# Optimization experiments

Hardware: AMD Instinct MI355X
Metric: run time of the kernel (lower is better)

Reference implementation:

```python
import jax, jax.numpy as jnp
import numpy as np

N = 50000   # num_nodes
D = 128     # h_dim
R = 32      # num_rels * 2 (forward + inverse relations)
B = 8       # num_bases
E = 600000  # num_edges


def setup_inputs() -> dict:
    key = jax.random.key(0)
    ks = jax.random.split(key, 14)
    s = 1.0 / np.sqrt(D)
    return {
        "h_ids": jnp.arange(N, dtype=jnp.int32),
        "src": jax.random.randint(ks[0], (E,), 0, N),
        "dst": jax.random.randint(ks[1], (E,), 0, N),
        "etype": jax.random.randint(ks[2], (E,), 0, R),
        "norm": jax.random.uniform(ks[3], (E, 1), dtype=jnp.float32),
        "embedding": jax.random.normal(ks[4], (N, D), dtype=jnp.float32) * 0.05,
        "w_comp1": jax.random.normal(ks[5], (R, B), dtype=jnp.float32) * (1.0 / np.sqrt(B)),
        "bases1": jax.random.normal(ks[6], (B, D, D), dtype=jnp.float32) * s,
        "loop_w1": jax.random.normal(ks[7], (D, D), dtype=jnp.float32) * s,
        "bias1": jnp.zeros((D,), dtype=jnp.float32),
        "w_comp2": jax.random.normal(ks[8], (R, B), dtype=jnp.float32) * (1.0 / np.sqrt(B)),
        "bases2": jax.random.normal(ks[9], (B, D, D), dtype=jnp.float32) * s,
        "loop_w2": jax.random.normal(ks[10], (D, D), dtype=jnp.float32) * s,
        "bias2": jnp.zeros((D,), dtype=jnp.float32),
    }


def _rel_graph_conv(h, src, dst, etype, norm, w_comp, bases, loop_w, bias, act):
    # basis decomposition: W[r] = sum_b w_comp[r,b] * bases[b]
    W = jnp.einsum('rb,bio->rio', w_comp, bases)          # [R, D, D]
    # transform every node by every relation weight (dense GEMM)
    all_t = jnp.einsum('ni,rio->nro', h, W)               # [N, R, D]
    # per-edge gather of relation-specific transformed source features
    msg = all_t[src, etype] * norm                        # [E, D]
    # scatter-aggregate messages at destination nodes
    agg = jax.ops.segment_sum(msg, dst, num_segments=h.shape[0])  # [N, D]
    out = agg + h @ loop_w + bias                         # self-loop + bias
    return act(out) if act is not None else out


def reference(h_ids, src, dst, etype, norm, embedding,
              w_comp1, bases1, loop_w1, bias1,
              w_comp2, bases2, loop_w2, bias2):
    # EmbeddingLayer
    h = embedding[h_ids]                                  # [N, D]
    # hidden layer 0: relu activation (idx < num_hidden_layers-1)
    h = _rel_graph_conv(h, src, dst, etype, norm, w_comp1, bases1, loop_w1, bias1, jax.nn.relu)
    # hidden layer 1: no activation (last layer)
    h = _rel_graph_conv(h, src, dst, etype, norm, w_comp2, bases2, loop_w2, bias2, None)
    return h
```

## Files before the change

kernel.cpp:

```cpp
#include <hip/hip_runtime.h>

#define DD 128
#define NB 8
#define KTOT 1152

typedef unsigned int uint_t;
typedef __attribute__((ext_vector_type(8))) _Float16 half8v;
typedef __attribute__((ext_vector_type(2))) _Float16 half2v;
typedef __attribute__((ext_vector_type(4))) float f32x4;

static __device__ __forceinline__ void gld_lds16(const _Float16* g, _Float16* l)
{
  __builtin_amdgcn_global_load_lds(
      (const __attribute__((address_space(1))) void*)g,
      (__attribute__((address_space(3))) void*)l, 16, 0, 0);
}

static __device__ __forceinline__ half2v bc_h2(uint_t u)
{
  union { uint_t u; half2v h; } c; c.u = u; return c.h;
}

static __device__ __forceinline__ float fdot2(uint_t a, uint_t b, float acc)
{
#if __has_builtin(__builtin_amdgcn_fdot2)
  return __builtin_amdgcn_fdot2(bc_h2(a), bc_h2(b), acc, false);
#else
  half2v x = bc_h2(a), y = bc_h2(b);
  return acc + (float)x[0] * (float)y[0] + (float)x[1] * (float)y[1];
#endif
}

__global__ __launch_bounds__(256) void k_prep_w(
    const float* __restrict__ bases1, const float* __restrict__ loopw1,
    const float* __restrict__ bases2, const float* __restrict__ loopw2,
    _Float16* __restrict__ WcA)
{
  int i = blockIdx.x * 256 + threadIdx.x;
  if (i >= 2 * 36 * DD * 32) return;
  int layer = i / (36 * DD * 32);
  int rem   = i % (36 * DD * 32);
  int ks    = rem / (DD * 32);
  int rem2  = rem % (DD * 32);
  int feat  = rem2 / 32;
  int j     = rem2 % 32;
  int k     = ks * 32 + j;
  const float* basesL = layer ? bases2 : bases1;
  const float* loopwL = layer ? loopw2 : loopw1;
  float v;
  if (k < 1024) {
    int kk = k >> 3, b = k & 7;
    v = basesL[((size_t)b * DD + kk) * DD + feat];
  } else {
    v = loopwL[(size_t)(k - 1024) * DD + feat];
  }
  WcA[i] = (_Float16)v;
}

__global__ __launch_bounds__(256) void k_cast(
    const float* __restrict__ h, const int* __restrict__ ids,
    _Float16* __restrict__ hf, int N)
{
  int i = blockIdx.x * 256 + threadIdx.x;
  if (i >= N * (DD / 8)) return;
  int n  = i / (DD / 8);
  int k8 = (i % (DD / 8)) * 8;
  int row = ids ? ids[n] : n;
  const float* hp = h + (size_t)row * DD + k8;
  float4 v0 = *(const float4*)hp;
  float4 v1 = *(const float4*)(hp + 4);
  union { _Float16 e[8]; uint4 q; } p;
  p.e[0]=(_Float16)v0.x; p.e[1]=(_Float16)v0.y; p.e[2]=(_Float16)v0.z; p.e[3]=(_Float16)v0.w;
  p.e[4]=(_Float16)v1.x; p.e[5]=(_Float16)v1.y; p.e[6]=(_Float16)v1.z; p.e[7]=(_Float16)v1.w;
  *(uint4*)&hf[(size_t)n * DD + k8] = p.q;
}

__global__ __launch_bounds__(256) void k_zero(int* __restrict__ p, int n)
{
  int i = blockIdx.x * 256 + threadIdx.x;
  if (i < n) p[i] = 0;
}

__global__ __launch_bounds__(256) void k_fill(int* __restrict__ p, int val, int n)
{
  int i = blockIdx.x * 256 + threadIdx.x;
  if (i < n) p[i] = val;
}

__global__ __launch_bounds__(256) void k_hist(
    const int* __restrict__ dst, int* __restrict__ cnt, int E)
{
  int e = blockIdx.x * 256 + threadIdx.x;
  if (e < E) atomicAdd(&cnt[dst[e]], 1);
}

__global__ __launch_bounds__(256) void k_bsum(
    const int* __restrict__ cnt, int* __restrict__ bsum, int N)
{
  __shared__ int s[256];
  int i = blockIdx.x * 256 + threadIdx.x;
  s[threadIdx.x] = (i < N) ? ((cnt[i] + 1) & ~1) : 0;
  __syncthreads();
  for (int off = 128; off > 0; off >>= 1) {
    if (threadIdx.x < off) s[threadIdx.x] += s[threadIdx.x + off];
    __syncthreads();
  }
  if (threadIdx.x == 0) bsum[blockIdx.x] = s[0];
}

__global__ __launch_bounds__(256) void k_scanb(
    const int* __restrict__ bsum, int* __restrict__ boff, int nb)
{
  __shared__ int s[256];
  int t = threadIdx.x;
  int own = (t < nb) ? bsum[t] : 0;
  s[t] = own;
  __syncthreads();
  for (int off = 1; off < 256; off <<= 1) {
    int v = (t >= off) ? s[t - off] : 0;
    __syncthreads();
    s[t] += v;
    __syncthreads();
  }
  if (t < nb) boff[t] = s[t] - own;
}

__global__ __launch_bounds__(256) void k_scan3(
    const int* __restrict__ cnt, const int* __restrict__ boff,
    int* __restrict__ row_start, int N)
{
  __shared__ int s[256];
  int t = threadIdx.x;
  int i = blockIdx.x * 256 + t;
  int v = (i < N) ? ((cnt[i] + 1) & ~1) : 0;
  s[t] = v;
  __syncthreads();
  for (int off = 1; off < 256; off <<= 1) {
    int u = (t >= off) ? s[t - off] : 0;
    __syncthreads();
    s[t] += u;
    __syncthreads();
  }
  if (i < N) row_start[i] = boff[blockIdx.x] + s[t] - v;
}

__global__ __launch_bounds__(256) void k_place(
    const int* __restrict__ dst, const int* __restrict__ row_start,
    int* __restrict__ cursor, int* __restrict__ perm, int E)
{
  int e = blockIdx.x * 256 + threadIdx.x;
  if (e < E) {
    int v = dst[e];
    int slot = row_start[v] + atomicAdd(&cursor[v], 1);
    perm[slot] = e;
  }
}

__global__ __launch_bounds__(256) void k_payload_pair(
    const int* __restrict__ perm, const int* __restrict__ src,
    const int* __restrict__ etype, const float* __restrict__ norm,
    const float* __restrict__ wcomp1, const float* __restrict__ wcomp2,
    int* __restrict__ psrc, _Float16* __restrict__ c1, _Float16* __restrict__ c2,
    int npair)
{
  int i = blockIdx.x * 256 + threadIdx.x;
  if (i >= npair) return;
  int e0 = perm[2 * i], e1 = perm[2 * i + 1];

  int s0 = 0, s1 = 0;
  float n0 = 0.f, n1 = 0.f;
  const float *w10 = wcomp1, *w20 = wcomp2, *w11 = wcomp1, *w21 = wcomp2;
  if (e0 >= 0) { s0 = src[e0]; n0 = norm[e0]; int t = etype[e0]; w10 = wcomp1 + t * NB; w20 = wcomp2 + t * NB; }
  if (e1 >= 0) { s1 = src[e1]; n1 = norm[e1]; int t = etype[e1]; w11 = wcomp1 + t * NB; w21 = wcomp2 + t * NB; }

  *(int2*)&psrc[2 * i] = make_int2(s0, s1);

  union { _Float16 h[16]; uint4 q[2]; } p;
  #pragma unroll
  for (int b = 0; b < NB; b++) {
    p.h[b * 2]     = (_Float16)(w10[b] * n0);
    p.h[b * 2 + 1] = (_Float16)(w11[b] * n1);
  }
  *(uint4*)&c1[(size_t)i * 16]     = p.q[0];
  *(uint4*)&c1[(size_t)i * 16 + 8] = p.q[1];
  #pragma unroll
  for (int b = 0; b < NB; b++) {
    p.h[b * 2]     = (_Float16)(w20[b] * n0);
    p.h[b * 2 + 1] = (_Float16)(w21[b] * n1);
  }
  *(uint4*)&c2[(size_t)i * 16]     = p.q[0];
  *(uint4*)&c2[(size_t)i * 16 + 8] = p.q[1];
}

__global__ __launch_bounds__(256) void k_agg(
    const int* __restrict__ rowst, const int* __restrict__ cnt,
    const int* __restrict__ psrc, const _Float16* __restrict__ cpair,
    const _Float16* __restrict__ hf,
    _Float16* __restrict__ agg, int N)
{
  int v = blockIdx.x * 4 + (threadIdx.x >> 6);
  if (v >= N) return;
  int lane = threadIdx.x & 63;
  const uint_t* hf32 = (const uint_t*)hf;
  const int beg = rowst[v];
  const int npairs = (cnt[v] + 1) >> 1;
  const uint_t* cp = (const uint_t*)cpair + (size_t)(beg >> 1) * 8;
  const int* ps = psrc + beg;

  float ax[NB] = {}, ay[NB] = {};
  int i = 0;
  for (; i + 2 <= npairs; i += 2) {
    int s0 = ps[2*i + 0], s1 = ps[2*i + 1];
    int s2 = ps[2*i + 2], s3 = ps[2*i + 3];
    uint_t u0 = hf32[(size_t)s0 * 64 + lane];
    uint_t u1 = hf32[(size_t)s1 * 64 + lane];
    uint_t u2 = hf32[(size_t)s2 * 64 + lane];
    uint_t u3 = hf32[(size_t)s3 * 64 + lane];
    uint_t lo01 = __builtin_amdgcn_perm(u0, u1, 0x01000504);
    uint_t hi01 = __builtin_amdgcn_perm(u0, u1, 0x03020706);
    uint_t lo23 = __builtin_amdgcn_perm(u2, u3, 0x01000504);
    uint_t hi23 = __builtin_amdgcn_perm(u2, u3, 0x03020706);
    #pragma unroll
    for (int b = 0; b < NB; b++) {
      uint_t ca = cp[(size_t)i * 8 + b];
      uint_t cb = cp[(size_t)(i + 1) * 8 + b];
      ax[b] = fdot2(ca, lo01, ax[b]);
      ay[b] = fdot2(ca, hi01, ay[b]);
      ax[b] = fdot2(cb, lo23, ax[b]);
      ay[b] = fdot2(cb, hi23, ay[b]);
    }
  }
  if (i < npairs) {
    int s0 = ps[2*i + 0], s1 = ps[2*i + 1];
    uint_t u0 = hf32[(size_t)s0 * 64 + lane];
    uint_t u1 = hf32[(size_t)s1 * 64 + lane];
    uint_t lo01 = __builtin_amdgcn_perm(u0, u1, 0x01000504);
    uint_t hi01 = __builtin_amdgcn_perm(u0, u1, 0x03020706);
    #pragma unroll
    for (int b = 0; b < NB; b++) {
      uint_t ca = cp[(size_t)i * 8 + b];
      ax[b] = fdot2(ca, lo01, ax[b]);
      ay[b] = fdot2(ca, hi01, ay[b]);
    }
  }

  union { _Float16 e[8]; uint4 q; } p0, p1;
  #pragma unroll
  for (int b = 0; b < NB; b++) { p0.e[b] = (_Float16)ax[b]; p1.e[b] = (_Float16)ay[b]; }
  uint4* dstp = (uint4*)&agg[(size_t)v * 1024 + lane * 16];
  dstp[0] = p0.q;
  dstp[1] = p1.q;
}

template <int LAYER>
__global__ __launch_bounds__(256) void k_mm(
    const _Float16* __restrict__ agg,
    const _Float16* __restrict__ hf,
    const _Float16* __restrict__ WcA,
    const float* __restrict__ bias,
    float* __restrict__ outf, _Float16* __restrict__ outh, int N)
{
  __shared__ _Float16 sB[2][4096];

  const int n0   = blockIdx.x * 64;
  const int wv   = threadIdx.x >> 6;
  const int lane = threadIdx.x & 63;
  const int l15  = lane & 15, l4 = lane >> 4;

  int nodeL = n0 + lane; if (nodeL >= N) nodeL = N - 1;

  f32x4 acc[2][4];
  #pragma unroll
  for (int a = 0; a < 2; a++)
    #pragma unroll
    for (int b = 0; b < 4; b++) acc[a][b] = (f32x4)0.f;

  const int fbase = wv * 32 + l15;
  const int koff  = l4 * 8;

  auto STAGE = [&](int buf, int t) {
    const _Float16 *g0, *g1;
    if (t < 16) {
      g0 = &agg[(size_t)nodeL * 1024 + (2 * t)     * 32 + wv * 8];
      g1 = &agg[(size_t)nodeL * 1024 + (2 * t + 1) * 32 + wv * 8];
    } else {
      g0 = &hf[(size_t)nodeL * DD + (2 * t - 32) * 32 + wv * 8];
      g1 = &hf[(size_t)nodeL * DD + (2 * t - 31) * 32 + wv * 8];
    }
    gld_lds16(g0, &sB[buf][ wv      * 512]);
    gld_lds16(g1, &sB[buf][(wv + 4) * 512]);
  };

  auto COMPUTE = [&](int buf, int t) {
    #pragma unroll
    for (int sub = 0; sub < 2; sub++) {
      const int ks = 2 * t + sub;
      half8v af[2], bfr[4];
      #pragma unroll
      for (int mf = 0; mf < 2; mf++)
        af[mf] = *(const half8v*)&WcA[((size_t)ks * DD + fbase + mf * 16) * 32 + koff];
      #pragma unroll
      for (int nf = 0; nf < 4; nf++)
        bfr[nf] = *(const half8v*)&sB[buf][(l4 + sub * 4) * 512 + (nf * 16 + l15) * 8];
      #pragma unroll
      for (int mf = 0; mf < 2; mf++)
        #pragma unroll
        for (int nf = 0; nf < 4; nf++)
          acc[mf][nf] = __builtin_amdgcn_mfma_f32_16x16x32_f16(af[mf], bfr[nf], acc[mf][nf], 0, 0, 0);
    }
  };

  STAGE(0, 0);
  __syncthreads();
  int cur = 0;
  for (int t = 0; t < 17; t++) {
    STAGE(cur ^ 1, t + 1);
    COMPUTE(cur, t);
    __syncthreads();
    cur ^= 1;
  }
  COMPUTE(cur, 17);

  #pragma unroll
  for (int mf = 0; mf < 2; mf++)
    #pragma unroll
    for (int nf = 0; nf < 4; nf++) {
      int n = n0 + nf * 16 + l15;
      if (n >= N) continue;
      int feat = wv * 32 + mf * 16 + l4 * 4;
      if (LAYER == 1) {
        union { _Float16 e[4]; uint2 q; } p;
        #pragma unroll
        for (int r = 0; r < 4; r++)
          p.e[r] = (_Float16)fmaxf(acc[mf][nf][r] + bias[feat + r], 0.f);
        *(uint2*)&outh[(size_t)n * DD + feat] = p.q;
      } else {
        float4 o;
        o.x = acc[mf][nf][0] + bias[feat + 0];
        o.y = acc[mf][nf][1] + bias[feat + 1];
        o.z = acc[mf][nf][2] + bias[feat + 2];
        o.w = acc[mf][nf][3] + bias[feat + 3];
        *(float4*)&outf[(size_t)n * DD + feat] = o;
      }
    }
}

extern "C" void kernel_launch(void* const* d_in, const int* in_sizes, int n_in,
                              void* d_out, int out_size, void* d_ws, size_t ws_size,
                              hipStream_t stream)
{
  const int*   h_ids     = (const int*)d_in[0];
  const int*   src       = (const int*)d_in[1];
  const int*   dst       = (const int*)d_in[2];
  const int*   etype     = (const int*)d_in[3];
  const float* norm      = (const float*)d_in[4];
  const float* embedding = (const float*)d_in[5];
  const float* w_comp1   = (const float*)d_in[6];
  const float* bases1    = (const float*)d_in[7];
  const float* loop_w1   = (const float*)d_in[8];
  const float* bias1     = (const float*)d_in[9];
  const float* w_comp2   = (const float*)d_in[10];
  const float* bases2    = (const float*)d_in[11];
  const float* loop_w2   = (const float*)d_in[12];
  const float* bias2     = (const float*)d_in[13];

  const int N = in_sizes[0];
  const int E = in_sizes[1];
  const int S = (E + N) & ~1;
  const int NPAIR = S >> 1;
  const int NBLK = (N + 255) / 256;

  char* base = (char*)d_ws;
  size_t off = 0;
  auto alloc = [&](size_t bytes) -> char* {
    char* p = base + off;
    off += (bytes + 255) & ~(size_t)255;
    return p;
  };
  _Float16* agg  = (_Float16*)alloc((size_t)N * 1024 * 2);
  _Float16* hfp  = (_Float16*)alloc((size_t)N * DD * 2);
  _Float16* h1h  = (_Float16*)alloc((size_t)N * DD * 2);
  _Float16* WcA  = (_Float16*)alloc((size_t)2 * 36 * DD * 32 * 2);
  int*      cnt    = (int*)   alloc((size_t)2 * N * 4);
  int*      cursor = cnt + N;
  int*      rowst  = (int*)   alloc((size_t)N * 4);
  int*      bsum   = (int*)   alloc(256 * 4);
  int*      boff   = (int*)   alloc(256 * 4);
  int*      perm   = (int*)   alloc((size_t)S * 4);
  int*      psrc   = (int*)   alloc((size_t)S * 4);
  _Float16* c1     = (_Float16*)alloc((size_t)S * 8 * 2);
  _Float16* c2     = (_Float16*)alloc((size_t)S * 8 * 2);
  float*    out    = (float*)d_out;

  k_zero <<<(2 * N + 255) / 256, 256, 0, stream>>>(cnt, 2 * N);
  k_fill <<<(S + 255) / 256, 256, 0, stream>>>(perm, -1, S);
  k_hist <<<(E + 255) / 256, 256, 0, stream>>>(dst, cnt, E);
  k_bsum <<<NBLK, 256, 0, stream>>>(cnt, bsum, N);
  k_scanb<<<1, 256, 0, stream>>>(bsum, boff, NBLK);
  k_scan3<<<NBLK, 256, 0, stream>>>(cnt, boff, rowst, N);
  k_place<<<(E + 255) / 256, 256, 0, stream>>>(dst, rowst, cursor, perm, E);
  k_payload_pair<<<(NPAIR + 255) / 256, 256, 0, stream>>>(
      perm, src, etype, norm, w_comp1, w_comp2, psrc, c1, c2, NPAIR);

  k_prep_w<<<(2 * 36 * DD * 32 + 255) / 256, 256, 0, stream>>>(bases1, loop_w1, bases2, loop_w2, WcA);

  dim3 gmm((N + 63) / 64);
  int gagg = (N + 3) / 4;

  k_cast<<<(N * (DD / 8) + 255) / 256, 256, 0, stream>>>(embedding, h_ids, hfp, N);
  k_agg<<<gagg, 256, 0, stream>>>(rowst, cnt, psrc, c1, hfp, agg, N);
  k_mm<1><<<gmm, 256, 0, stream>>>(agg, hfp, WcA, bias1, nullptr, h1h, N);

  k_agg<<<gagg, 256, 0, stream>>>(rowst, cnt, psrc, c2, h1h, agg, N);
  k_mm<2><<<gmm, 256, 0, stream>>>(agg, h1h, WcA + (size_t)36 * DD * 32, bias2, out, nullptr, N);
}
```

Measured before the change: 276.2 us.

## Scatter edge payload directly in placement and drop LDS staging in node GEMM

Edge placement now writes the source id and packed (etype, norm) straight into CSR slots, so the payload kernel no longer performs indirect gathers through a permutation array. Padded slots are zero-filled in place of the old -1 sentinel, which gives them norm 0. The fused GEMM kernel drops the double-buffered LDS staging: each wave handles 16 nodes against all 128 output features, loading node rows directly from global memory and weights from global/L2. This removes LDS traffic and barriers, but each wave now rereads the full weight matrix and relies on caches for latency hiding.

```diff
diff --git a/kernel.cpp b/kernel.cpp
--- a/kernel.cpp
+++ b/kernel.cpp
@@ -8,13 +8,6 @@
 typedef __attribute__((ext_vector_type(8))) _Float16 half8v;
 typedef __attribute__((ext_vector_type(2))) _Float16 half2v;
 typedef __attribute__((ext_vector_type(4))) float f32x4;
-
-static __device__ __forceinline__ void gld_lds16(const _Float16* g, _Float16* l)
-{
-  __builtin_amdgcn_global_load_lds(
-      (const __attribute__((address_space(1))) void*)g,
-      (__attribute__((address_space(3))) void*)l, 16, 0, 0);
-}
 
 static __device__ __forceinline__ half2v bc_h2(uint_t u)
 {
@@ -81,12 +74,6 @@
   if (i < n) p[i] = 0;
 }
 
-__global__ __launch_bounds__(256) void k_fill(int* __restrict__ p, int val, int n)
-{
-  int i = blockIdx.x * 256 + threadIdx.x;
-  if (i < n) p[i] = val;
-}
-
 __global__ __launch_bounds__(256) void k_hist(
     const int* __restrict__ dst, int* __restrict__ cnt, int E)
 {
@@ -145,35 +132,33 @@
 }
 
 __global__ __launch_bounds__(256) void k_place(
-    const int* __restrict__ dst, const int* __restrict__ row_start,
-    int* __restrict__ cursor, int* __restrict__ perm, int E)
+    const int* __restrict__ dst, const int* __restrict__ src,
+    const int* __restrict__ etype, const float* __restrict__ norm,
+    const int* __restrict__ row_start, int* __restrict__ cursor,
+    int* __restrict__ psrc, int2* __restrict__ en, int E)
 {
   int e = blockIdx.x * 256 + threadIdx.x;
   if (e < E) {
     int v = dst[e];
     int slot = row_start[v] + atomicAdd(&cursor[v], 1);
-    perm[slot] = e;
+    psrc[slot] = src[e];
+    en[slot] = make_int2(etype[e], __float_as_int(norm[e]));
   }
 }
 
 __global__ __launch_bounds__(256) void k_payload_pair(
-    const int* __restrict__ perm, const int* __restrict__ src,
-    const int* __restrict__ etype, const float* __restrict__ norm,
+    const int2* __restrict__ en,
     const float* __restrict__ wcomp1, const float* __restrict__ wcomp2,
-    int* __restrict__ psrc, _Float16* __restrict__ c1, _Float16* __restrict__ c2,
-    int npair)
+    _Float16* __restrict__ c1, _Float16* __restrict__ c2, int npair)
 {
   int i = blockIdx.x * 256 + threadIdx.x;
   if (i >= npair) return;
-  int e0 = perm[2 * i], e1 = perm[2 * i + 1];
-
-  int s0 = 0, s1 = 0;
-  float n0 = 0.f, n1 = 0.f;
-  const float *w10 = wcomp1, *w20 = wcomp2, *w11 = wcomp1, *w21 = wcomp2;
-  if (e0 >= 0) { s0 = src[e0]; n0 = norm[e0]; int t = etype[e0]; w10 = wcomp1 + t * NB; w20 = wcomp2 + t * NB; }
-  if (e1 >= 0) { s1 = src[e1]; n1 = norm[e1]; int t = etype[e1]; w11 = wcomp1 + t * NB; w21 = wcomp2 + t * NB; }
-
-  *(int2*)&psrc[2 * i] = make_int2(s0, s1);
+  int2 e0 = en[2 * i], e1 = en[2 * i + 1];
+  float n0 = __int_as_float(e0.y), n1 = __int_as_float(e1.y);
+  const float* w10 = wcomp1 + e0.x * NB;
+  const float* w11 = wcomp1 + e1.x * NB;
+  const float* w20 = wcomp2 + e0.x * NB;
+  const float* w21 = wcomp2 + e1.x * NB;
 
   union { _Float16 h[16]; uint4 q[2]; } p;
   #pragma unroll
@@ -260,89 +245,60 @@
     const float* __restrict__ bias,
     float* __restrict__ outf, _Float16* __restrict__ outh, int N)
 {
-  __shared__ _Float16 sB[2][4096];
-
-  const int n0   = blockIdx.x * 64;
   const int wv   = threadIdx.x >> 6;
   const int lane = threadIdx.x & 63;
   const int l15  = lane & 15, l4 = lane >> 4;
-
-  int nodeL = n0 + lane; if (nodeL >= N) nodeL = N - 1;
-
-  f32x4 acc[2][4];
-  #pragma unroll
-  for (int a = 0; a < 2; a++)
-    #pragma unroll
-    for (int b = 0; b < 4; b++) acc[a][b] = (f32x4)0.f;
-
-  const int fbase = wv * 32 + l15;
-  const int koff  = l4 * 8;
-
-  auto STAGE = [&](int buf, int t) {
-    const _Float16 *g0, *g1;
-    if (t < 16) {
-      g0 = &agg[(size_t)nodeL * 1024 + (2 * t)     * 32 + wv * 8];
-      g1 = &agg[(size_t)nodeL * 1024 + (2 * t + 1) * 32 + wv * 8];
-    } else {
-      g0 = &hf[(size_t)nodeL * DD + (2 * t - 32) * 32 + wv * 8];
-      g1 = &hf[(size_t)nodeL * DD + (2 * t - 31) * 32 + wv * 8];
-    }
-    gld_lds16(g0, &sB[buf][ wv      * 512]);
-    gld_lds16(g1, &sB[buf][(wv + 4) * 512]);
-  };
-
-  auto COMPUTE = [&](int buf, int t) {
-    #pragma unroll
-    for (int sub = 0; sub < 2; sub++) {
-      const int ks = 2 * t + sub;
-      half8v af[2], bfr[4];
-      #pragma unroll
-      for (int mf = 0; mf < 2; mf++)
-        af[mf] = *(const half8v*)&WcA[((size_t)ks * DD + fbase + mf * 16) * 32 + koff];
-      #pragma unroll
-      for (int nf = 0; nf < 4; nf++)
-        bfr[nf] = *(const half8v*)&sB[buf][(l4 + sub * 4) * 512 + (nf * 16 + l15) * 8];
-      #pragma unroll
-      for (int mf = 0; mf < 2; mf++)
-        #pragma unroll
-        for (int nf = 0; nf < 4; nf++)
-          acc[mf][nf] = __builtin_amdgcn_mfma_f32_16x16x32_f16(af[mf], bfr[nf], acc[mf][nf], 0, 0, 0);
-    }
-  };
-
-  STAGE(0, 0);
-  __syncthreads();
-  int cur = 0;
-  for (int t = 0; t < 17; t++) {
-    STAGE(cur ^ 1, t + 1);
-    COMPUTE(cur, t);
-    __syncthreads();
-    cur ^= 1;
-  }
-  COMPUTE(cur, 17);
-
-  #pragma unroll
-  for (int mf = 0; mf < 2; mf++)
-    #pragma unroll
-    for (int nf = 0; nf < 4; nf++) {
-      int n = n0 + nf * 16 + l15;
-      if (n >= N) continue;
-      int feat = wv * 32 + mf * 16 + l4 * 4;
+  const int n0w  = blockIdx.x * 64 + wv * 16;
+
+  int node = n0w + l15; if (node >= N) node = N - 1;
+  const _Float16* brow = agg + (size_t)node * 1024;
+  const _Float16* hrow = hf  + (size_t)node * DD;
+  const int koff = l4 * 8;
+
+  f32x4 acc[8];
+  #pragma unroll
+  for (int mf = 0; mf < 8; mf++) acc[mf] = (f32x4)0.f;
+
+  #pragma unroll 2
+  for (int ks = 0; ks < 32; ks++) {
+    half8v bfr = *(const half8v*)&brow[ks * 32 + koff];
+    #pragma unroll
+    for (int mf = 0; mf < 8; mf++) {
+      half8v af = *(const half8v*)&WcA[((size_t)ks * DD + mf * 16 + l15) * 32 + koff];
+      acc[mf] = __builtin_amdgcn_mfma_f32_16x16x32_f16(af, bfr, acc[mf], 0, 0, 0);
+    }
+  }
+  #pragma unroll
+  for (int ks = 32; ks < 36; ks++) {
+    half8v bfr = *(const half8v*)&hrow[(ks - 32) * 32 + koff];
+    #pragma unroll
+    for (int mf = 0; mf < 8; mf++) {
+      half8v af = *(const half8v*)&WcA[((size_t)ks * DD + mf * 16 + l15) * 32 + koff];
+      acc[mf] = __builtin_amdgcn_mfma_f32_16x16x32_f16(af, bfr, acc[mf], 0, 0, 0);
+    }
+  }
+
+  int n = n0w + l15;
+  if (n < N) {
+    #pragma unroll
+    for (int mf = 0; mf < 8; mf++) {
+      int feat = mf * 16 + l4 * 4;
       if (LAYER == 1) {
         union { _Float16 e[4]; uint2 q; } p;
         #pragma unroll
         for (int r = 0; r < 4; r++)
-          p.e[r] = (_Float16)fmaxf(acc[mf][nf][r] + bias[feat + r], 0.f);
+          p.e[r] = (_Float16)fmaxf(acc[mf][r] + bias[feat + r], 0.f);
         *(uint2*)&outh[(size_t)n * DD + feat] = p.q;
       } else {
         float4 o;
-        o.x = acc[mf][nf][0] + bias[feat + 0];
-        o.y = acc[mf][nf][1] + bias[feat + 1];
-        o.z = acc[mf][nf][2] + bias[feat + 2];
-        o.w = acc[mf][nf][3] + bias[feat + 3];
+        o.x = acc[mf][0] + bias[feat + 0];
+        o.y = acc[mf][1] + bias[feat + 1];
+        o.z = acc[mf][2] + bias[feat + 2];
+        o.w = acc[mf][3] + bias[feat + 3];
         *(float4*)&outf[(size_t)n * DD + feat] = o;
       }
     }
+  }
 }
 
 extern "C" void kernel_launch(void* const* d_in, const int* in_sizes, int n_in,
@@ -386,21 +342,23 @@
   int*      rowst  = (int*)   alloc((size_t)N * 4);
   int*      bsum   = (int*)   alloc(256 * 4);
   int*      boff   = (int*)   alloc(256 * 4);
-  int*      perm   = (int*)   alloc((size_t)S * 4);
   int*      psrc   = (int*)   alloc((size_t)S * 4);
+  int2*     en     = (int2*)  alloc((size_t)S * 8);
   _Float16* c1     = (_Float16*)alloc((size_t)S * 8 * 2);
   _Float16* c2     = (_Float16*)alloc((size_t)S * 8 * 2);
   float*    out    = (float*)d_out;
 
   k_zero <<<(2 * N + 255) / 256, 256, 0, stream>>>(cnt, 2 * N);
-  k_fill <<<(S + 255) / 256, 256, 0, stream>>>(perm, -1, S);
+  k_zero <<<(S + 255) / 256, 256, 0, stream>>>(psrc, S);
+  k_zero <<<(2 * S + 255) / 256, 256, 0, stream>>>((int*)en, 2 * S);
   k_hist <<<(E + 255) / 256, 256, 0, stream>>>(dst, cnt, E);
   k_bsum <<<NBLK, 256, 0, stream>>>(cnt, bsum, N);
   k_scanb<<<1, 256, 0, stream>>>(bsum, boff, NBLK);
   k_scan3<<<NBLK, 256, 0, stream>>>(cnt, boff, rowst, N);
-  k_place<<<(E + 255) / 256, 256, 0, stream>>>(dst, rowst, cursor, perm, E);
+  k_place<<<(E + 255) / 256, 256, 0, stream>>>(dst, src, etype, norm,
+                                               rowst, cursor, psrc, en, E);
   k_payload_pair<<<(NPAIR + 255) / 256, 256, 0, stream>>>(
-      perm, src, etype, norm, w_comp1, w_comp2, psrc, c1, c2, NPAIR);
+      en, w_comp1, w_comp2, c1, c2, NPAIR);
 
   k_prep_w<<<(2 * 36 * DD * 32 + 255) / 256, 256, 0, stream>>>(bases1, loop_w1, bases2, loop_w2, WcA);
 
```

Result: slower. 364.3 us (+31.9%).
